# Optimization experiments

Hardware: AMD Instinct MI355X
Metric: run time of the kernel (lower is better)

Reference implementation:

```python
import math
import jax, jax.numpy as jnp
import numpy as np

# ---- static configuration (mirrors init_kwargs / chosen shapes) ----
MUL = 16          # multiplicity in "16x0e+16x1e+16x2e"
B_CFG = 64        # number of configurations in batch
N_ATOM = 64       # atoms per configuration
N_NODES = B_CFG * N_ATOM
N_PAIRS = B_CFG * N_ATOM * N_ATOM

# ---- real Wigner 3j symbols (e3nn convention), computed once in numpy ----
def _su2_cg(j1, m1, j2, m2, j3, m3):
    if m3 != m1 + m2:
        return 0.0
    f = math.factorial
    vmin = max(-j1 + j2 + m3, -j1 + m1, 0)
    vmax = min(j2 + j3 + m1, j3 - j1 + j2, j3 + m3)
    C = math.sqrt((2 * j3 + 1) * f(j3 + j1 - j2) * f(j3 - j1 + j2) * f(j1 + j2 - j3)
                  * f(j3 + m3) * f(j3 - m3)
                  / (f(j1 + j2 + j3 + 1) * f(j1 - m1) * f(j1 + m1) * f(j2 - m2) * f(j2 + m2)))
    S = 0.0
    for v in range(vmin, vmax + 1):
        S += (-1) ** (v + j2 + m2) * f(j2 + j3 + m1 - v) * f(j1 - m1 + v) / (
            f(v) * f(j3 - j1 + j2 - v) * f(j3 + m3 - v) * f(v + j1 - j2 - m3))
    return C * S

def _q_real_to_complex(l):
    q = np.zeros((2 * l + 1, 2 * l + 1), dtype=np.complex128)
    for m in range(-l, 0):
        q[l + m, l + abs(m)] = 1 / 2 ** 0.5
        q[l + m, l - abs(m)] = -1j / 2 ** 0.5
    q[l, l] = 1.0
    for m in range(1, l + 1):
        q[l + m, l + abs(m)] = (-1) ** m / 2 ** 0.5
        q[l + m, l - abs(m)] = 1j * (-1) ** m / 2 ** 0.5
    return (-1j) ** l * q

def _wigner_3j(l1, l2, l3):
    C = np.zeros((2 * l1 + 1, 2 * l2 + 1, 2 * l3 + 1))
    for m1 in range(-l1, l1 + 1):
        for m2 in range(-l2, l2 + 1):
            m3 = m1 + m2
            if abs(m3) <= l3:
                C[l1 + m1, l2 + m2, l3 + m3] = _su2_cg(l1, m1, l2, m2, l3, m3)
    Q1, Q2, Q3 = _q_real_to_complex(l1), _q_real_to_complex(l2), _q_real_to_complex(l3)
    Cr = np.einsum('ij,kl,mn,ikm->jln', Q1, Q2, np.conj(Q3), C.astype(np.complex128))
    assert np.abs(Cr.imag).max() < 1e-6
    Cr = Cr.real
    return Cr / np.linalg.norm(Cr)

# all CG paths (l1, l2, l_out) of the fully connected TP (0e+1e+2e)^2 -> 0e+1e+2e
PATHS = [(0, 0, 0), (1, 1, 0), (2, 2, 0),
         (0, 1, 1), (1, 0, 1), (1, 1, 1), (1, 2, 1), (2, 1, 1), (2, 2, 1),
         (0, 2, 2), (2, 0, 2), (1, 1, 2), (1, 2, 2), (2, 1, 2), (2, 2, 2)]
W3J = {p: _wigner_3j(*p) for p in set(PATHS)}
FAN = {lo: sum(1 for p in PATHS if p[2] == lo) * MUL * MUL for lo in (0, 1, 2)}
ALPHA = {lo: math.sqrt(2 * lo + 1) / math.sqrt(FAN[lo]) for lo in (0, 1, 2)}
# CartesianTensor('ij=ij') change of basis: x_ij = sum_{l,m} QCART[lm,i,j] * irreps[lm]
QCART = np.concatenate([math.sqrt(2 * l + 1) * np.transpose(_wigner_3j(1, 1, l), (2, 0, 1))
                        for l in (0, 1, 2)], axis=0)  # (9, 3, 3), orthonormal rows


def setup_inputs() -> dict:
    key = jax.random.key(0)
    k1, k2 = jax.random.split(key)
    node_feats = jax.random.normal(k1, (N_NODES, MUL * 9), dtype=jnp.float32)
    # layout: for each config, all (i, j) atom pairs with global node indices
    ii, jj = jnp.meshgrid(jnp.arange(N_ATOM, dtype=jnp.int32),
                          jnp.arange(N_ATOM, dtype=jnp.int32), indexing='ij')
    base = (jnp.arange(B_CFG, dtype=jnp.int32) * N_ATOM)[:, None, None]
    rows = (base + ii[None]).reshape(-1)
    cols = (base + jj[None]).reshape(-1)
    layout = jnp.stack([rows, cols], axis=1)  # (N_PAIRS, 2) int32
    tp_weights = jax.random.normal(k2, (len(PATHS), MUL, MUL), dtype=jnp.float32)
    return {'node_feats': node_feats, 'layout': layout, 'tp_weights': tp_weights}


def _split(x):
    # (E, MUL*9) -> {l: (E, MUL, 2l+1)} in irreps order 16x0e | 16x1e | 16x2e
    E = x.shape[0]
    return {0: x[:, :MUL].reshape(E, MUL, 1),
            1: x[:, MUL:4 * MUL].reshape(E, MUL, 3),
            2: x[:, 4 * MUL:].reshape(E, MUL, 5)}


def _forward(node_feats, tp_weights, layout):
    x1 = _split(node_feats[layout[:, 0]])   # gather row atoms
    x2 = _split(node_feats[layout[:, 1]])   # gather column atoms
    E = layout.shape[0]
    dt = node_feats.dtype
    out = {lo: jnp.zeros((E, 2 * lo + 1), dt) for lo in (0, 1, 2)}
    for p, (l1, l2, lo) in enumerate(PATHS):
        w3j = jnp.asarray(W3J[(l1, l2, lo)], dt)
        t = jnp.einsum('eui,uv->evi', x1[l1], tp_weights[p])          # mix multiplicities
        out[lo] = out[lo] + ALPHA[lo] * jnp.einsum('evi,evj,ijk->ek', t, x2[l2], w3j)
    irr = jnp.concatenate([out[0], out[1], out[2]], axis=1)           # (E, 9) = 0e+1e+2e
    cart = jnp.einsum('ek,kij->eij', irr, jnp.asarray(QCART, dt))     # (E, 3, 3)
    # symmetrize: (H + H^T)/2 on the 3n x 3n per-config Hessian
    c = cart.reshape(B_CFG, N_ATOM, N_ATOM, 3, 3)
    c = 0.5 * (c + jnp.transpose(c, (0, 2, 1, 4, 3)))
    return c.reshape(E, 3, 3)


def reference(node_feats, layout, tp_weights):
    return _forward(node_feats, tp_weights, layout)
```

## Files before the change

### kernel.cpp

```cpp
#include <hip/hip_runtime.h>
#include <math.h>


#define NPATH 15

constexpr double cfact(int n){ double r = 1.0; for (int i = 2; i <= n; ++i) r *= (double)i; return r; }
constexpr double csqrt(double x){
  if (x <= 0.0) return 0.0;
  double g = x < 1.0 ? 1.0 : x;
  for (int i = 0; i < 64; ++i) g = 0.5*(g + x/g);
  return g;
}

constexpr double ccg(int j1,int m1,int j2,int m2,int j3,int m3){
  if (m3 != m1 + m2) return 0.0;
  int vmin = -j1 + j2 + m3;
  if (-j1 + m1 > vmin) vmin = -j1 + m1;
  if (0 > vmin) vmin = 0;
  int vmax = j2 + j3 + m1;
  if (j3 - j1 + j2 < vmax) vmax = j3 - j1 + j2;
  if (j3 + m3 < vmax) vmax = j3 + m3;
  double C = csqrt((2.0*j3+1.0)*cfact(j3+j1-j2)*cfact(j3-j1+j2)*cfact(j1+j2-j3)
                   *cfact(j3+m3)*cfact(j3-m3)
                   /(cfact(j1+j2+j3+1)*cfact(j1-m1)*cfact(j1+m1)*cfact(j2-m2)*cfact(j2+m2)));
  double S = 0.0;
  for (int v = vmin; v <= vmax; ++v){
    double term = cfact(j2+j3+m1-v)*cfact(j1-m1+v)
                /(cfact(v)*cfact(j3-j1+j2-v)*cfact(j3+m3-v)*cfact(v+j1-j2-m3));
    S += ((v + j2 + m2) & 1) ? -term : term;
  }
  return C * S;
}

struct QM { double re[5][5]; double im[5][5]; };
constexpr QM cbuild_q(int l){
  QM q{};
  double s = 1.0 / csqrt(2.0);
  for (int m = -l; m < 0; ++m){
    q.re[l+m][l-m] = s;
    q.im[l+m][l+m] = -s;
  }
  q.re[l][l] = 1.0;
  for (int m = 1; m <= l; ++m){
    double sg = (m & 1) ? -1.0 : 1.0;
    q.re[l+m][l+m] = sg * s;
    q.im[l+m][l-m] = sg * s;
  }
  if (l == 1){
    for (int r = 0; r < 5; ++r)
      for (int c = 0; c < 5; ++c){
        double a = q.re[r][c], b = q.im[r][c];
        q.re[r][c] = b; q.im[r][c] = -a;
      }
  } else if (l == 2){
    for (int r = 0; r < 5; ++r)
      for (int c = 0; c < 5; ++c){ q.re[r][c] = -q.re[r][c]; q.im[r][c] = -q.im[r][c]; }
  }
  return q;
}

struct CRP { double v[125]; };
constexpr CRP make_cr(int l1, int l2, int l3){
  QM q1 = cbuild_q(l1), q2 = cbuild_q(l2), q3 = cbuild_q(l3);
  const int d1 = 2*l1+1, d2 = 2*l2+1, d3 = 2*l3+1;
  double CG[125] = {};
  for (int i = 0; i < d1; ++i)
    for (int k = 0; k < d2; ++k)
      for (int m = 0; m < d3; ++m)
        CG[(i*5 + k)*5 + m] = ccg(l1, i-l1, l2, k-l2, l3, m-l3);
  CRP o{};
  for (int j = 0; j < d1; ++j)
    for (int l = 0; l < d2; ++l)
      for (int n = 0; n < d3; ++n){
        double acc = 0.0;
        for (int i = 0; i < d1; ++i)
          for (int k = 0; k < d2; ++k)
            for (int m = 0; m < d3; ++m){
              double c = CG[(i*5 + k)*5 + m];
              if (c == 0.0) continue;
              double are = q1.re[i][j], aim = q1.im[i][j];
              double bre = q2.re[k][l], bim = q2.im[k][l];
              double tre = are*bre - aim*bim;
              double tim = are*bim + aim*bre;
              double cre = q3.re[m][n], cim = q3.im[m][n];
              acc += (tre*cre + tim*cim) * c;
            }
        o.v[(j*d2 + l)*d3 + n] = acc;
      }
  double s2 = 0.0;
  for (int e = 0; e < d1*d2*d3; ++e) s2 += o.v[e]*o.v[e];
  double inv = 1.0 / csqrt(s2);
  for (int e = 0; e < d1*d2*d3; ++e) o.v[e] *= inv;
  return o;
}

constexpr CRP CR0  = make_cr(0,0,0);
constexpr CRP CR1  = make_cr(1,1,0);
constexpr CRP CR2  = make_cr(2,2,0);
constexpr CRP CR3  = make_cr(0,1,1);
constexpr CRP CR4  = make_cr(1,0,1);
constexpr CRP CR5  = make_cr(1,1,1);
constexpr CRP CR6  = make_cr(1,2,1);
constexpr CRP CR7  = make_cr(2,1,1);
constexpr CRP CR8  = make_cr(2,2,1);
constexpr CRP CR9  = make_cr(0,2,2);
constexpr CRP CR10 = make_cr(2,0,2);
constexpr CRP CR11 = make_cr(1,1,2);
constexpr CRP CR12 = make_cr(1,2,2);
constexpr CRP CR13 = make_cr(2,1,2);
constexpr CRP CR14 = make_cr(2,2,2);

struct QCT { double v[81]; };
constexpr QCT make_qc(){
  QCT q{};
  for (int lm = 0; lm < 9; ++lm){
    int l = (lm == 0) ? 0 : ((lm < 4) ? 1 : 2);
    int m = lm - l*l;
    const CRP& cr = (l == 0) ? CR1 : ((l == 1) ? CR5 : CR11);
    double sc = csqrt(2.0*l + 1.0);
    for (int r = 0; r < 9; ++r)
      q.v[lm*9 + r] = cr.v[r*(2*l+1) + m] * sc;
  }
  return q;
}
constexpr QCT QCt = make_qc();

struct WQT { float b8[189*8]; float b1[189]; };
constexpr WQT make_wq(){
  WQT t{};
  const CRP* crs[NPATH] = {&CR0,&CR1,&CR2,&CR3,&CR4,&CR5,&CR6,&CR7,&CR8,&CR9,
                           &CR10,&CR11,&CR12,&CR13,&CR14};
  const int L1[NPATH]   = {0,1,2,0,1,1,1,2,2,0,2,1,1,2,2};
  const int L2[NPATH]   = {0,1,2,1,0,1,2,1,2,2,0,1,2,1,2};
  const int LO[NPATH]   = {0,0,0,1,1,1,1,1,1,2,2,2,2,2,2};
  const int PROW[NPATH] = {0,1,10,35,38,41,50,65,80,105,110,115,124,139,164};
  const double AL[3] = { csqrt(1.0/768.0), csqrt(3.0/1536.0), csqrt(5.0/1536.0) };
  for (int p = 0; p < NPATH; ++p){
    const int d1 = 2*L1[p]+1, d2 = 2*L2[p]+1, d3 = 2*LO[p]+1, lo = LO[p];
    for (int i = 0; i < d1; ++i)
      for (int j = 0; j < d2; ++j)
        for (int a = 0; a < 9; ++a){
          double acc = 0.0;
          for (int m = 0; m < d3; ++m)
            acc += crs[p]->v[(i*d2 + j)*d3 + m] * QCt.v[(lo*lo + m)*9 + a];
          double val = AL[lo] * acc;
          int row = PROW[p] + i*d2 + j;
          if (a < 8) t.b8[row*8 + a] = (float)val;
          else       t.b1[row]       = (float)val;
        }
  }
  return t;
}
__constant__ WQT cWQ = make_wq();

__constant__ int cP_L1[NPATH]   = {0,1,2,0,1,1,1,2,2,0,2,1,1,2,2};
__constant__ int cC2P[51] = {0, 1,1,1, 2,2,2,2,2, 3, 4,4,4, 5,5,5, 6,6,6,
                             7,7,7,7,7, 8,8,8,8,8, 9, 10,10,10,10,10,
                             11,11,11, 12,12,12, 13,13,13,13,13, 14,14,14,14,14};
__constant__ int cC2I[51] = {0, 0,1,2, 0,1,2,3,4, 0, 0,1,2, 0,1,2, 0,1,2,
                             0,1,2,3,4, 0,1,2,3,4, 0, 0,1,2,3,4,
                             0,1,2, 0,1,2, 0,1,2,3,4, 0,1,2,3,4};

#define ACCP(TOFF_, PROW_, D1_)                                              \
  { _Pragma("unroll")                                                        \
    for (int i = 0; i < (D1_); ++i){                                         \
      float tv = pT[((TOFF_) + i) * 16 + v];                                 \
      int row = (PROW_) + i * D2 + j;                                        \
      const float4 m0 = *(const float4*)&sB8[row * 8];                       \
      const float4 m1 = *(const float4*)&sB8[row * 8 + 4];                   \
      const float  m8 = sB1[row];                                            \
      acc[0] += tv*m0.x; acc[1] += tv*m0.y; acc[2] += tv*m0.z;               \
      acc[3] += tv*m0.w; acc[4] += tv*m1.x; acc[5] += tv*m1.y;               \
      acc[6] += tv*m1.z; acc[7] += tv*m1.w; acc[8] += tv*m8;                 \
    } }

__global__ __launch_bounds__(256, 2) void fused8_kernel(
    const float* __restrict__ feats,
    const int*   __restrict__ layout,
    const float* __restrict__ tpw,
    float*       __restrict__ out)
{
  __shared__ __align__(16) float U[11776];
  __shared__ __align__(16) float sMq[4][1728];
  __shared__ __align__(16) float sX1T[4][192];
  __shared__ int sCol[64];
  __shared__ int sMeta[51];

  const int tid  = threadIdx.x;
  const int wave = tid >> 6;
  const int lane = tid & 63;
  const int rwBase = blockIdx.x * 4;
  const int rw = rwBase + wave;

  float* sB8   = U;
  float* sB1   = U + 1512;
  float* sTPWT = U + 4968;

  for (int o = tid; o < 1512; o += 256) sB8[o] = cWQ.b8[o];
  if (tid < 189) sB1[tid] = cWQ.b1[tid];
  for (int e = tid; e < 3840; e += 256){
    int p = e >> 8, r = e & 255, u = r >> 4, v = r & 15;
    sTPWT[p * 324 + v * 20 + u] = tpw[e];
  }
  if (tid < 51){
    int p = cC2P[tid], i = cC2I[tid], l1 = cP_L1[p];
    int xb = (l1 == 0) ? 0 : ((l1 == 1) ? 16 + i * 20 : 80 + i * 20);
    sMeta[tid] = xb | ((p * 324) << 16);
  }
  if (tid >= 192)
    sCol[tid - 192] = layout[2 * ((size_t)rwBase * 64 + (tid - 192)) + 1];

  {
    int rn = layout[2 * (rw * 64)];
    rn = __builtin_amdgcn_readfirstlane(rn);
    const float* g = feats + (size_t)rn * 144;
    float* xt = sX1T[wave];
    if (lane < 16) xt[lane] = g[lane];
    if (lane < 48){ int i = lane >> 4, u = lane & 15;
      xt[16 + i * 20 + u] = g[16 + u * 3 + i]; }
    { int i = lane >> 4, u = lane & 15;
      xt[80 + i * 20 + u] = g[64 + u * 5 + i]; }
    if (lane < 16) xt[160 + lane] = g[64 + lane * 5 + 4];
  }
  __syncthreads();

  float* pT = U + 1704 + wave * 816;
  {
    const int v  = lane & 15;
    const int cq = lane >> 4;
    const float* xw = sX1T[wave];
    #pragma unroll
    for (int it = 0; it < 13; ++it){
      int c = cq + it * 4;
      if (c < 51){
        int md = sMeta[c];
        const float* xb = xw + (md & 0xffff);
        const float* wb = sTPWT + (md >> 16) + v * 20;
        float s = 0.f;
        #pragma unroll
        for (int u4 = 0; u4 < 4; ++u4){
          float4 xv = *(const float4*)(xb + u4 * 4);
          float4 wv = *(const float4*)(wb + u4 * 4);
          s += xv.x * wv.x; s += xv.y * wv.y;
          s += xv.z * wv.z; s += xv.w * wv.w;
        }
        pT[c * 16 + v] = s;
      }
    }
  }

  float* pM = sMq[wave];
  for (int rnd = 0; rnd < 3; ++rnd){
    int c = lane + rnd * 64;
    if (c >= 144) break;
    float acc[9];
    #pragma unroll
    for (int a = 0; a < 9; ++a) acc[a] = 0.f;
    if (c < 16){
      const int v = c, j = 0;
      const int D2 = 1;
      ACCP(0,  0,   1)
      ACCP(10, 38,  3)
      ACCP(30, 110, 5)
    } else if (c < 64){
      const int v = (c - 16) / 3, j = (c - 16) % 3;
      const int D2 = 3;
      ACCP(1,  1,   3)
      ACCP(9,  35,  1)
      ACCP(13, 41,  3)
      ACCP(19, 65,  5)
      ACCP(35, 115, 3)
      ACCP(41, 139, 5)
    } else {
      const int v = (c - 64) / 5, j = (c - 64) % 5;
      const int D2 = 5;
      ACCP(4,  10,  5)
      ACCP(16, 50,  3)
      ACCP(24, 80,  5)
      ACCP(29, 105, 1)
      ACCP(38, 124, 3)
      ACCP(46, 164, 5)
    }
    *(float4*)&pM[c * 12]     = make_float4(acc[0], acc[1], acc[2], acc[3]);
    *(float4*)&pM[c * 12 + 4] = make_float4(acc[4], acc[5], acc[6], acc[7]);
    pM[c * 12 + 8] = acc[8];
  }
  __syncthreads();

  float* sX2R = U;
  #pragma unroll
  for (int k = 0; k < 9; ++k){
    int q = k * 256 + tid;
    int j = q / 36, c4 = q - j * 36;
    const float4 xv = *(const float4*)(feats + (size_t)sCol[j] * 144 + c4 * 4);
    *(float4*)(sX2R + j * 148 + c4 * 4) = xv;
  }
  __syncthreads();

  const float* xrow = sX2R + lane * 148;
  float acc[9];
  #pragma unroll
  for (int a = 0; a < 9; ++a) acc[a] = 0.f;

  #pragma unroll 4
  for (int c4 = 0; c4 < 36; ++c4){
    float4 xv = *(const float4*)(xrow + c4 * 4);
    #pragma unroll
    for (int r = 0; r < 4; ++r){
      int c = c4 * 4 + r;
      float xs = (r == 0) ? xv.x : ((r == 1) ? xv.y : ((r == 2) ? xv.z : xv.w));
      const float4 m0 = *(const float4*)&pM[c * 12];
      const float4 m1 = *(const float4*)&pM[c * 12 + 4];
      const float  m8 = pM[c * 12 + 8];
      acc[0] += xs * m0.x; acc[1] += xs * m0.y; acc[2] += xs * m0.z;
      acc[3] += xs * m0.w; acc[4] += xs * m1.x; acc[5] += xs * m1.y;
      acc[6] += xs * m1.z; acc[7] += xs * m1.w; acc[8] += xs * m8;
    }
  }

  float* pO = U + 9472 + wave * 576;
  #pragma unroll
  for (int a = 0; a < 9; ++a) pO[lane * 9 + a] = acc[a];
  float* ob = out + (size_t)rw * 576;
  #pragma unroll
  for (int r = 0; r < 3; ++r){
    int idx = lane + r * 64;
    if (idx < 144){
      float4 vv = *(const float4*)(pO + idx * 4);
      *(float4*)(ob + idx * 4) = vv;
    }
  }
}

__global__ __launch_bounds__(256) void sym_tiled(float* __restrict__ out){
  __shared__ float sA[16 * 145];
  __shared__ float sB[16 * 145];
  const int tid = threadIdx.x;
  const int b  = blockIdx.x / 10;
  const int tp = blockIdx.x - b * 10;
  const int TI[10] = {0,0,0,0,1,1,1,2,2,3};
  const int TJ[10] = {0,1,2,3,1,2,3,2,3,3};
  const int ti = TI[tp], tj = TJ[tp];
  const bool diag = (ti == tj);
  const size_t cfgBase = (size_t)b * 4096 * 9;

  for (int idx = tid; idx < 2304; idx += 256){
    int r = idx / 144, off = idx - r * 144;
    sA[r * 145 + off] = out[cfgBase + ((size_t)(ti*16 + r) * 64 + tj*16) * 9 + off];
  }
  if (!diag){
    for (int idx = tid; idx < 2304; idx += 256){
      int r = idx / 144, off = idx - r * 144;
      sB[r * 145 + off] = out[cfgBase + ((size_t)(tj*16 + r) * 64 + ti*16) * 9 + off];
    }
  }
  __syncthreads();

  const int di = tid >> 4, dj = tid & 15;
  const float* A = sA;
  const float* B = diag ? sA : sB;
  float oa[9], ob[9];
  #pragma unroll
  for (int a = 0; a < 3; ++a)
    #pragma unroll
    for (int d = 0; d < 3; ++d){
      oa[a*3+d] = 0.5f * (A[di*145 + dj*9 + a*3+d] + B[dj*145 + di*9 + d*3+a]);
      if (!diag)
        ob[a*3+d] = 0.5f * (B[di*145 + dj*9 + a*3+d] + A[dj*145 + di*9 + d*3+a]);
    }
  __syncthreads();

  #pragma unroll
  for (int r9 = 0; r9 < 9; ++r9) sA[di*145 + dj*9 + r9] = oa[r9];
  if (!diag){
    #pragma unroll
    for (int r9 = 0; r9 < 9; ++r9) sB[di*145 + dj*9 + r9] = ob[r9];
  }
  __syncthreads();

  for (int idx = tid; idx < 2304; idx += 256){
    int r = idx / 144, off = idx - r * 144;
    out[cfgBase + ((size_t)(ti*16 + r) * 64 + tj*16) * 9 + off] = sA[r * 145 + off];
  }
  if (!diag){
    for (int idx = tid; idx < 2304; idx += 256){
      int r = idx / 144, off = idx - r * 144;
      out[cfgBase + ((size_t)(tj*16 + r) * 64 + ti*16) * 9 + off] = sB[r * 145 + off];
    }
  }
}

extern "C" void kernel_launch(void* const* d_in, const int* in_sizes, int n_in,
                              void* d_out, int out_size, void* d_ws, size_t ws_size,
                              hipStream_t stream) {
  const float* feats  = (const float*)d_in[0];
  const int*   layout = (const int*)  d_in[1];
  const float* tpw    = (const float*)d_in[2];
  float* out = (float*)d_out;
  (void)d_ws; (void)ws_size; (void)n_in; (void)out_size;

  const int E = in_sizes[1] / 2;
  const int R = E / 64;
  const int B = E / 4096;

  fused8_kernel<<<R / 4, 256, 0, stream>>>(feats, layout, tpw, out);
  sym_tiled<<<B * 10, 256, 0, stream>>>(out);
}
```

Measured before the change: 112.8 us.

## Shrink shared memory, read column features directly from global, transpose M layout

Packs the shared-memory buffers into one smaller overlaid region so three blocks fit per CU instead of two. The M matrix is stored transposed (component-major) so the inner loop can use float4 loads across four channels. The column-feature staging pass and its barriers are removed, so each lane reads its column atom's features straight from global memory. The risks are uncoalesced per-lane global loads (each lane reads a different 576-byte row) and register pressure under the tighter launch bound.

```diff
diff --git a/kernel.cpp b/kernel.cpp
--- a/kernel.cpp
+++ b/kernel.cpp
@@ -161,6 +161,13 @@
                              0,1,2,3,4, 0,1,2,3,4, 0, 0,1,2,3,4,
                              0,1,2, 0,1,2, 0,1,2,3,4, 0,1,2,3,4};
 
+#define WQ8_OFF  0
+#define WQ1_OFF  1512
+#define PT_OFF   1704
+#define OVR_OFF  4968
+#define X1T_OFF  10152
+#define U_SIZE   10920
+
 #define ACCP(TOFF_, PROW_, D1_)                                              \
   { _Pragma("unroll")                                                        \
     for (int i = 0; i < (D1_); ++i){                                         \
@@ -174,15 +181,13 @@
       acc[6] += tv*m1.z; acc[7] += tv*m1.w; acc[8] += tv*m8;                 \
     } }
 
-__global__ __launch_bounds__(256, 2) void fused8_kernel(
+__global__ __launch_bounds__(256, 3) void fused9_kernel(
     const float* __restrict__ feats,
     const int*   __restrict__ layout,
     const float* __restrict__ tpw,
     float*       __restrict__ out)
 {
-  __shared__ __align__(16) float U[11776];
-  __shared__ __align__(16) float sMq[4][1728];
-  __shared__ __align__(16) float sX1T[4][192];
+  __shared__ __align__(16) float U[U_SIZE];
   __shared__ int sCol[64];
   __shared__ int sMeta[51];
 
@@ -192,9 +197,9 @@
   const int rwBase = blockIdx.x * 4;
   const int rw = rwBase + wave;
 
-  float* sB8   = U;
-  float* sB1   = U + 1512;
-  float* sTPWT = U + 4968;
+  float* sB8   = U + WQ8_OFF;
+  float* sB1   = U + WQ1_OFF;
+  float* sTPWT = U + OVR_OFF;
 
   for (int o = tid; o < 1512; o += 256) sB8[o] = cWQ.b8[o];
   if (tid < 189) sB1[tid] = cWQ.b1[tid];
@@ -214,7 +219,7 @@
     int rn = layout[2 * (rw * 64)];
     rn = __builtin_amdgcn_readfirstlane(rn);
     const float* g = feats + (size_t)rn * 144;
-    float* xt = sX1T[wave];
+    float* xt = U + X1T_OFF + wave * 192;
     if (lane < 16) xt[lane] = g[lane];
     if (lane < 48){ int i = lane >> 4, u = lane & 15;
       xt[16 + i * 20 + u] = g[16 + u * 3 + i]; }
@@ -224,11 +229,11 @@
   }
   __syncthreads();
 
-  float* pT = U + 1704 + wave * 816;
+  float* pT = U + PT_OFF + wave * 816;
   {
     const int v  = lane & 15;
     const int cq = lane >> 4;
-    const float* xw = sX1T[wave];
+    const float* xw = U + X1T_OFF + wave * 192;
     #pragma unroll
     for (int it = 0; it < 13; ++it){
       int c = cq + it * 4;
@@ -248,8 +253,9 @@
       }
     }
   }
-
-  float* pM = sMq[wave];
+  __syncthreads();
+
+  float* pMq = U + OVR_OFF + wave * 1296;
   for (int rnd = 0; rnd < 3; ++rnd){
     int c = lane + rnd * 64;
     if (c >= 144) break;
@@ -281,53 +287,41 @@
       ACCP(38, 124, 3)
       ACCP(46, 164, 5)
     }
-    *(float4*)&pM[c * 12]     = make_float4(acc[0], acc[1], acc[2], acc[3]);
-    *(float4*)&pM[c * 12 + 4] = make_float4(acc[4], acc[5], acc[6], acc[7]);
-    pM[c * 12 + 8] = acc[8];
-  }
-  __syncthreads();
-
-  float* sX2R = U;
-  #pragma unroll
-  for (int k = 0; k < 9; ++k){
-    int q = k * 256 + tid;
-    int j = q / 36, c4 = q - j * 36;
-    const float4 xv = *(const float4*)(feats + (size_t)sCol[j] * 144 + c4 * 4);
-    *(float4*)(sX2R + j * 148 + c4 * 4) = xv;
-  }
-  __syncthreads();
-
-  const float* xrow = sX2R + lane * 148;
-  float acc[9];
-  #pragma unroll
-  for (int a = 0; a < 9; ++a) acc[a] = 0.f;
-
-  #pragma unroll 4
-  for (int c4 = 0; c4 < 36; ++c4){
-    float4 xv = *(const float4*)(xrow + c4 * 4);
-    #pragma unroll
-    for (int r = 0; r < 4; ++r){
-      int c = c4 * 4 + r;
-      float xs = (r == 0) ? xv.x : ((r == 1) ? xv.y : ((r == 2) ? xv.z : xv.w));
-      const float4 m0 = *(const float4*)&pM[c * 12];
-      const float4 m1 = *(const float4*)&pM[c * 12 + 4];
-      const float  m8 = pM[c * 12 + 8];
-      acc[0] += xs * m0.x; acc[1] += xs * m0.y; acc[2] += xs * m0.z;
-      acc[3] += xs * m0.w; acc[4] += xs * m1.x; acc[5] += xs * m1.y;
-      acc[6] += xs * m1.z; acc[7] += xs * m1.w; acc[8] += xs * m8;
-    }
-  }
-
-  float* pO = U + 9472 + wave * 576;
-  #pragma unroll
-  for (int a = 0; a < 9; ++a) pO[lane * 9 + a] = acc[a];
-  float* ob = out + (size_t)rw * 576;
-  #pragma unroll
-  for (int r = 0; r < 3; ++r){
-    int idx = lane + r * 64;
-    if (idx < 144){
-      float4 vv = *(const float4*)(pO + idx * 4);
-      *(float4*)(ob + idx * 4) = vv;
+    #pragma unroll
+    for (int a = 0; a < 9; ++a) pMq[a * 144 + c] = acc[a];
+  }
+
+  {
+    const int myCol = sCol[lane];
+    const float* xg = feats + (size_t)myCol * 144;
+    float acc[9];
+    #pragma unroll
+    for (int a = 0; a < 9; ++a) acc[a] = 0.f;
+
+    #pragma unroll 6
+    for (int c4 = 0; c4 < 36; ++c4){
+      float4 xv = *(const float4*)(xg + c4 * 4);
+      #pragma unroll
+      for (int a = 0; a < 9; ++a){
+        const float4 m = *(const float4*)&pMq[a * 144 + c4 * 4];
+        acc[a] += xv.x * m.x;
+        acc[a] += xv.y * m.y;
+        acc[a] += xv.z * m.z;
+        acc[a] += xv.w * m.w;
+      }
+    }
+
+    float* pO = U + PT_OFF + wave * 816;
+    #pragma unroll
+    for (int a = 0; a < 9; ++a) pO[lane * 9 + a] = acc[a];
+    float* ob = out + (size_t)rw * 576;
+    #pragma unroll
+    for (int r = 0; r < 3; ++r){
+      int idx = lane + r * 64;
+      if (idx < 144){
+        float4 vv = *(const float4*)(pO + idx * 4);
+        *(float4*)(ob + idx * 4) = vv;
+      }
     }
   }
 }
@@ -403,6 +397,6 @@
   const int R = E / 64;
   const int B = E / 4096;
 
-  fused8_kernel<<<R / 4, 256, 0, stream>>>(feats, layout, tpw, out);
+  fused9_kernel<<<R / 4, 256, 0, stream>>>(feats, layout, tpw, out);
   sym_tiled<<<B * 10, 256, 0, stream>>>(out);
 }
```

Result: slower. 119.9 us (+6.3%).
